# Optimization experiments

Measured on AMD Instinct MI355X. Metric: run time of the kernel, lower is better.

The kernel has to match this reference:

```python
import jax, jax.numpy as jnp
import numpy as np

N, QLEN, KLEN = 4, 2048, 2048
QDIM = KVDIM = 512
EMBED, HEADS = 1024, 16
HEAD_DIM = EMBED // HEADS


def setup_inputs() -> dict:
    key = jax.random.key(0)
    ks = jax.random.split(key, 7)
    return {
        "queries": jax.random.normal(ks[0], (N, QLEN, QDIM), dtype=jnp.float32),
        "keys": jax.random.normal(ks[1], (1, KLEN, KVDIM), dtype=jnp.float32),
        "values": jax.random.normal(ks[2], (1, KLEN, KVDIM), dtype=jnp.float32),
        "mask": jax.random.randint(ks[3], (N, 1, 1, KLEN), 0, 2, dtype=jnp.int32),
        "Wq": jax.random.normal(ks[4], (QDIM, EMBED), dtype=jnp.float32) * (QDIM ** -0.5),
        "Wk": jax.random.normal(ks[5], (KVDIM, EMBED), dtype=jnp.float32) * (KVDIM ** -0.5),
        "Wv": jax.random.normal(ks[6], (KVDIM, EMBED), dtype=jnp.float32) * (KVDIM ** -0.5),
    }


def reference(queries, keys, values, mask, Wq, Wk, Wv):
    # Projections (Linear, no bias)
    q = (queries @ Wq).reshape(N, QLEN, HEADS, HEAD_DIM)      # [N, Q, H, D]
    k = (keys @ Wk).reshape(KLEN, HEADS, HEAD_DIM)            # [K, H, D] (batch-1, shared)
    v = (values @ Wv).reshape(KLEN, HEADS, HEAD_DIM)          # [K, H, D]

    # energy: [N, H, Q, K]
    energy = jnp.einsum('nqhd,khd->nhqk', q, k)
    energy = jnp.where(mask == 0, jnp.float32(-1e20), energy)
    attn = jax.nn.softmax(energy / jnp.float32(HEAD_DIM ** 0.5), axis=3)

    out = jnp.einsum('nhqk,khd->nqhd', attn, v)               # [N, Q, H, D]
    return out.reshape(N, QLEN, EMBED)
```

## Files before the change

kernel.cpp:

```cpp
#include <hip/hip_runtime.h>

#define NB 4
#define QLEN 2048
#define KLEN 2048
#define QDIM 512
#define EMBED 1024
#define HEADS 16
#define HD 64

typedef __bf16 bf16x8 __attribute__((ext_vector_type(8)));
typedef float f32x4 __attribute__((ext_vector_type(4)));
typedef float f32x16 __attribute__((ext_vector_type(16)));

#define CLOG 0.18033688011112042f

__device__ __forceinline__ float fexp2(float x) {
#if __has_builtin(__builtin_amdgcn_exp2f)
    return __builtin_amdgcn_exp2f(x);
#else
    float r;
    asm("v_exp_f32 %0, %1\n\ts_nop 1" : "=v"(r) : "v"(x));
    return r;
#endif
}

#if __has_builtin(__builtin_amdgcn_sched_barrier)
#define SCHED_FENCE() __builtin_amdgcn_sched_barrier(0)
#else
#define SCHED_FENCE()
#endif

__device__ __forceinline__ void dma16(const void* g, void* l) {
    __builtin_amdgcn_global_load_lds(
        (const __attribute__((address_space(1))) void*)g,
        (__attribute__((address_space(3))) void*)l, 16, 0, 0);
}

__global__ __launch_bounds__(256) void prep(const float* __restrict__ q,
                                            const float* __restrict__ k,
                                            const float* __restrict__ v,
                                            const float* __restrict__ Wq,
                                            const float* __restrict__ Wk,
                                            const float* __restrict__ Wv,
                                            __bf16* __restrict__ qd,
                                            __bf16* __restrict__ kd,
                                            __bf16* __restrict__ vd,
                                            __bf16* __restrict__ WtQ,
                                            __bf16* __restrict__ WtK,
                                            __bf16* __restrict__ WtV) {
    __shared__ float tile[32][33];
    int b = blockIdx.x, tid = threadIdx.x;
    if (b < 3072) {
        const float* src; __bf16* dst; int cb;
        if (b < 2048)      { src = q; dst = qd; cb = b; }
        else if (b < 2560) { src = k; dst = kd; cb = b - 2048; }
        else               { src = v; dst = vd; cb = b - 2560; }
        int i = (cb * 256 + tid) * 8;
        float4 a0 = *(const float4*)&src[i];
        float4 a1 = *(const float4*)&src[i + 4];
        bf16x8 o;
        o[0] = (__bf16)a0.x; o[1] = (__bf16)a0.y; o[2] = (__bf16)a0.z; o[3] = (__bf16)a0.w;
        o[4] = (__bf16)a1.x; o[5] = (__bf16)a1.y; o[6] = (__bf16)a1.z; o[7] = (__bf16)a1.w;
        *(bf16x8*)&dst[i] = o;
    } else {
        int tb = b - 3072;
        int which = tb >> 9, r = tb & 511;
        const float* src = (which == 0) ? Wq : (which == 1) ? Wk : Wv;
        __bf16* dst = (which == 0) ? WtQ : (which == 1) ? WtK : WtV;
        float scale = (which == 0) ? CLOG : 1.0f;
        int e0 = (r & 31) * 32, c0 = (r >> 5) * 32;
        int tx = tid & 31, ty = tid >> 5;
        for (int i = 0; i < 4; i++)
            tile[ty + 8 * i][tx] = src[(c0 + ty + 8 * i) * EMBED + e0 + tx];
        __syncthreads();
        for (int i = 0; i < 4; i++)
            dst[(e0 + ty + 8 * i) * QDIM + c0 + tx] = (__bf16)(tile[tx][ty + 8 * i] * scale);
    }
}

__device__ __forceinline__ void gemm_compute(const __bf16* As, const __bf16* Bs,
                                             int wr, int wc, int r16, int qq,
                                             f32x4 (&acc)[4][4]) {
    bf16x8 af[4], bq[4];
#pragma unroll
    for (int i = 0; i < 4; i++)
        af[i] = *(const bf16x8*)&As[(wr * 64 + i * 16 + r16) * 32 + qq * 8];
#pragma unroll
    for (int j = 0; j < 4; j++)
        bq[j] = *(const bf16x8*)&Bs[(wc * 64 + j * 16 + r16) * 32 + qq * 8];
#pragma unroll
    for (int i = 0; i < 4; i++)
#pragma unroll
        for (int j = 0; j < 4; j++)
            acc[i][j] = __builtin_amdgcn_mfma_f32_16x16x32_bf16(af[i], bq[j], acc[i][j], 0, 0, 0);
}

__device__ __forceinline__ void gemm128(const __bf16* __restrict__ A,
                                        const __bf16* __restrict__ Bt,
                                        __bf16* As0, __bf16* As1,
                                        __bf16* Bs0, __bf16* Bs1,
                                        int row0, int col0, f32x4 (&acc)[4][4]) {
    int tid = threadIdx.x, wave = tid >> 6, lane = tid & 63;
    int r16 = lane & 15, qq = lane >> 4;
    int wr = wave >> 1, wc = wave & 1;
    const __bf16* agp1 = A + (size_t)(row0 + (tid >> 2)) * QDIM + (tid & 3) * 8;
    const __bf16* agp2 = A + (size_t)(row0 + 64 + (tid >> 2)) * QDIM + (tid & 3) * 8;
    const __bf16* bgp1 = Bt + (size_t)(col0 + (tid >> 2)) * QDIM + (tid & 3) * 8;
    const __bf16* bgp2 = Bt + (size_t)(col0 + 64 + (tid >> 2)) * QDIM + (tid & 3) * 8;
    __bf16 *a0a = &As0[wave * 512], *a0b = &As0[2048 + wave * 512];
    __bf16 *a1a = &As1[wave * 512], *a1b = &As1[2048 + wave * 512];
    __bf16 *b0a = &Bs0[wave * 512], *b0b = &Bs0[2048 + wave * 512];
    __bf16 *b1a = &Bs1[wave * 512], *b1b = &Bs1[2048 + wave * 512];

    dma16(agp1, a0a); dma16(agp2, a0b);
    dma16(bgp1, b0a); dma16(bgp2, b0b);
    agp1 += 32; agp2 += 32; bgp1 += 32; bgp2 += 32;
    __syncthreads();

    for (int t = 0; t < 16; t += 2) {
        dma16(agp1, a1a); dma16(agp2, a1b);
        dma16(bgp1, b1a); dma16(bgp2, b1b);
        agp1 += 32; agp2 += 32; bgp1 += 32; bgp2 += 32;
        SCHED_FENCE();
        gemm_compute(As0, Bs0, wr, wc, r16, qq, acc);
        __syncthreads();
        if (t + 2 < 16) {
            dma16(agp1, a0a); dma16(agp2, a0b);
            dma16(bgp1, b0a); dma16(bgp2, b0b);
            agp1 += 32; agp2 += 32; bgp1 += 32; bgp2 += 32;
        }
        SCHED_FENCE();
        gemm_compute(As1, Bs1, wr, wc, r16, qq, acc);
        __syncthreads();
    }
}

__global__ __launch_bounds__(256) void proj_all(const __bf16* __restrict__ qin,
                                                const __bf16* __restrict__ kin,
                                                const __bf16* __restrict__ vin,
                                                const __bf16* __restrict__ wtq,
                                                const __bf16* __restrict__ wtk,
                                                const __bf16* __restrict__ wtv,
                                                __bf16* __restrict__ qout,
                                                __bf16* __restrict__ kout,
                                                __bf16* __restrict__ vtout) {
    __shared__ __align__(16) __bf16 As[2][128 * 32];
    __shared__ __align__(16) __bf16 Bs[2][128 * 32];
    int bid = blockIdx.x;
    const __bf16 *A, *Bt;
    int mode, b;
    if (bid < 512)      { A = qin; Bt = wtq; mode = 0; b = bid; }
    else if (bid < 640) { A = kin; Bt = wtk; mode = 1; b = bid - 512; }
    else                { A = vin; Bt = wtv; mode = 2; b = bid - 640; }
    int row0 = (b >> 3) * 128, col0 = (b & 7) * 128;
    f32x4 acc[4][4] = {};
    gemm128(A, Bt, As[0], As[1], Bs[0], Bs[1], row0, col0, acc);
    int lane = threadIdx.x & 63, wave = threadIdx.x >> 6;
    int r16 = lane & 15, qq = lane >> 4;
    int wr = wave >> 1, wc = wave & 1;
#pragma unroll
    for (int i = 0; i < 4; i++)
#pragma unroll
        for (int j = 0; j < 4; j++)
#pragma unroll
            for (int rr = 0; rr < 4; rr++) {
                int grow = row0 + wr * 64 + i * 16 + qq * 4 + rr;
                int gcol = col0 + wc * 64 + j * 16 + r16;
                int hh = gcol >> 6, d = gcol & 63;
                __bf16 v = (__bf16)acc[i][j][rr];
                if (mode == 0) {
                    int n = grow >> 11, qr = grow & 2047;
                    qout[((size_t)(n * HEADS + hh) * QLEN + qr) * HD + d] = v;
                } else if (mode == 1) {
                    kout[((size_t)hh * KLEN + grow) * HD + d] = v;
                } else {
                    vtout[((size_t)hh * HD + d) * KLEN + grow] = v;
                }
            }
}

__device__ __forceinline__ void attn_tile(const __bf16* ksb, const __bf16* vsb,
                                          const float* mrow, const bf16x8 (&qfrag)[4],
                                          int col, int h,
                                          f32x16& o0, f32x16& o1, float& rsl) {
    bf16x8 pfrag[4];
#pragma unroll
    for (int kt2 = 0; kt2 < 2; kt2++) {
        int R = kt2 * 32 + col;
        f32x16 s = {};
#pragma unroll
        for (int c = 0; c < 4; c++) {
            int cc = (2 * c + h) ^ (R & 7);
            bf16x8 kf = *(const bf16x8*)&ksb[(R * 8 + cc) * 8];
            s = __builtin_amdgcn_mfma_f32_32x32x16_bf16(kf, qfrag[c], s, 0, 0, 0);
        }
#pragma unroll
        for (int G = 0; G < 4; G++) {
            f32x4 mt = *(const f32x4*)&mrow[kt2 * 32 + 16 * (G >> 1) + 8 * h + 4 * (G & 1)];
            int ci = 2 * kt2 + (G >> 1), e0 = (G & 1) * 4;
#pragma unroll
            for (int rr = 0; rr < 4; rr++) {
                float p = fexp2(s[4 * G + rr] + mt[rr]);
                rsl += p;
                pfrag[ci][e0 + rr] = (__bf16)p;
            }
        }
    }
#pragma unroll
    for (int c = 0; c < 4; c++) {
        int cc = (2 * c + h) ^ (col & 7);
        bf16x8 v0 = *(const bf16x8*)&vsb[(col * 8 + cc) * 8];
        bf16x8 v1 = *(const bf16x8*)&vsb[((32 + col) * 8 + cc) * 8];
        o0 = __builtin_amdgcn_mfma_f32_32x32x16_bf16(v0, pfrag[c], o0, 0, 0, 0);
        o1 = __builtin_amdgcn_mfma_f32_32x32x16_bf16(v1, pfrag[c], o1, 0, 0, 0);
    }
}

__global__ __launch_bounds__(256, 4) void attn_kernel(const __bf16* __restrict__ qb,
                                                      const __bf16* __restrict__ kb,
                                                      const __bf16* __restrict__ vtb,
                                                      const int* __restrict__ mask,
                                                      float* __restrict__ out) {
    __shared__ __align__(16) __bf16 ks[2][4096];
    __shared__ __align__(16) __bf16 vs[2][4096];
    __shared__ __align__(16) float msf[KLEN];

    int tid = threadIdx.x, wave = tid >> 6, lane = tid & 63;
    int col = lane & 31, h = lane >> 5;
    int q0 = blockIdx.x * 128, hh = blockIdx.y, n = blockIdx.z;
    const __bf16* qg = qb + ((size_t)(n * HEADS + hh) * QLEN + q0 + wave * 32 + col) * HD;
    const __bf16* kg = kb + (size_t)hh * KLEN * HD;
    const __bf16* vg = vtb + (size_t)hh * HD * KLEN;
    const int* mg = mask + n * KLEN;

    bf16x8 qfrag[4];
#pragma unroll
    for (int c = 0; c < 4; c++) qfrag[c] = *(const bf16x8*)&qg[c * 16 + h * 8];

    int s1 = tid, R1 = s1 >> 3, c1 = (s1 & 7) ^ (R1 & 7);
    int s2 = tid + 256, R2 = s2 >> 3, c2 = (s2 & 7) ^ (R2 & 7);
    int g1 = (R1 & 0x33) | ((R1 & 4) << 1) | ((R1 & 8) >> 1);
    int g2 = (R2 & 0x33) | ((R2 & 4) << 1) | ((R2 & 8) >> 1);
    const __bf16* kgp1 = kg + g1 * HD + c1 * 8;
    const __bf16* kgp2 = kg + g2 * HD + c2 * 8;
    const __bf16* vgp1 = vg + (size_t)R1 * KLEN + c1 * 8;
    const __bf16* vgp2 = vg + (size_t)R2 * KLEN + c2 * 8;
    __bf16 *kl0a = &ks[0][wave * 512], *kl0b = &ks[0][2048 + wave * 512];
    __bf16 *kl1a = &ks[1][wave * 512], *kl1b = &ks[1][2048 + wave * 512];
    __bf16 *vl0a = &vs[0][wave * 512], *vl0b = &vs[0][2048 + wave * 512];
    __bf16 *vl1a = &vs[1][wave * 512], *vl1b = &vs[1][2048 + wave * 512];

    dma16(kgp1, kl0a); dma16(kgp2, kl0b);
    dma16(vgp1, vl0a); dma16(vgp2, vl0b);
    kgp1 += 64 * HD; kgp2 += 64 * HD; vgp1 += 64; vgp2 += 64;
    {
        int i8 = tid * 8;
        int4 ma = *(const int4*)&mg[i8];
        int4 mb = *(const int4*)&mg[i8 + 4];
        f32x4 fa, fb;
        fa[0] = ma.x ? 0.f : -1e30f; fa[1] = ma.y ? 0.f : -1e30f;
        fa[2] = ma.z ? 0.f : -1e30f; fa[3] = ma.w ? 0.f : -1e30f;
        fb[0] = mb.x ? 0.f : -1e30f; fb[1] = mb.y ? 0.f : -1e30f;
        fb[2] = mb.z ? 0.f : -1e30f; fb[3] = mb.w ? 0.f : -1e30f;
        *(f32x4*)&msf[i8] = fa;
        *(f32x4*)&msf[i8 + 4] = fb;
    }
    __syncthreads();

    f32x16 o0 = {}, o1 = {};
    float rsl = 0.f;

    for (int t = 0; t < 32; t += 2) {
        dma16(kgp1, kl1a); dma16(kgp2, kl1b);
        dma16(vgp1, vl1a); dma16(vgp2, vl1b);
        kgp1 += 64 * HD; kgp2 += 64 * HD; vgp1 += 64; vgp2 += 64;
        SCHED_FENCE();
        attn_tile(ks[0], vs[0], &msf[t * 64], qfrag, col, h, o0, o1, rsl);
        __syncthreads();
        if (t + 2 < 32) {
            dma16(kgp1, kl0a); dma16(kgp2, kl0b);
            dma16(vgp1, vl0a); dma16(vgp2, vl0b);
            kgp1 += 64 * HD; kgp2 += 64 * HD; vgp1 += 64; vgp2 += 64;
        }
        SCHED_FENCE();
        attn_tile(ks[1], vs[1], &msf[(t + 1) * 64], qfrag, col, h, o0, o1, rsl);
        __syncthreads();
    }

    rsl += __shfl_xor(rsl, 32);
    float inv = 1.0f / rsl;
    float* op = out + ((size_t)n * QLEN + q0 + wave * 32 + col) * EMBED + hh * HD;
#pragma unroll
    for (int G = 0; G < 4; G++) {
        float4 t0, t1;
        t0.x = o0[4 * G + 0] * inv; t0.y = o0[4 * G + 1] * inv;
        t0.z = o0[4 * G + 2] * inv; t0.w = o0[4 * G + 3] * inv;
        t1.x = o1[4 * G + 0] * inv; t1.y = o1[4 * G + 1] * inv;
        t1.z = o1[4 * G + 2] * inv; t1.w = o1[4 * G + 3] * inv;
        *(float4*)&op[8 * G + 4 * h] = t0;
        *(float4*)&op[32 + 8 * G + 4 * h] = t1;
    }
}

extern "C" void kernel_launch(void* const* d_in, const int* in_sizes, int n_in,
                              void* d_out, int out_size, void* d_ws, size_t ws_size,
                              hipStream_t stream) {
    const float* queries = (const float*)d_in[0];
    const float* keys    = (const float*)d_in[1];
    const float* values  = (const float*)d_in[2];
    const int*   mask    = (const int*)d_in[3];
    const float* Wq      = (const float*)d_in[4];
    const float* Wk      = (const float*)d_in[5];
    const float* Wv      = (const float*)d_in[6];
    float* out = (float*)d_out;

    const size_t MiB = 1048576;
    char* ws = (char*)d_ws;
    __bf16* qbf   = (__bf16*)(ws);
    __bf16* kbf   = (__bf16*)(ws + 16 * MiB);
    __bf16* vtbf  = (__bf16*)(ws + 20 * MiB);
    __bf16* wtq   = (__bf16*)(ws + 24 * MiB);
    __bf16* wtk   = (__bf16*)(ws + 25 * MiB);
    __bf16* wtv   = (__bf16*)(ws + 26 * MiB);
    __bf16* qin   = (__bf16*)(ws + 27 * MiB);
    __bf16* kin   = (__bf16*)(ws + 35 * MiB);
    __bf16* vin   = (__bf16*)(ws + 37 * MiB);

    prep<<<4608, 256, 0, stream>>>(queries, keys, values, Wq, Wk, Wv,
                                   qin, kin, vin, wtq, wtk, wtv);
    proj_all<<<768, 256, 0, stream>>>(qin, kin, vin, wtq, wtk, wtv, qbf, kbf, vtbf);
    attn_kernel<<<dim3(QLEN / 128, HEADS, NB), 256, 0, stream>>>(qbf, kbf, vtbf, mask, out);
}
```

Before: 193.5 us.

## Compute V projection transposed directly, fold mask into MFMA init, add setprio

The V projection GEMM swaps its operands (Wv^T times values^T) so the output tile is already in the transposed head layout and can be written with contiguous stores, replacing the scattered transposing writes. In attention, the mask bias is loaded into the score accumulator before the QK MFMAs, removing the per-element add before exp2. Row sums are accumulated as packed 2-wide floats, and s_setprio raises wave priority around the MFMA sections. The risk is that the V path depends on gemm128 producing the correct layout with swapped operands and a changed grid tiling, and that setprio may not help scheduling.

```diff
diff --git a/kernel.cpp b/kernel.cpp
--- a/kernel.cpp
+++ b/kernel.cpp
@@ -9,6 +9,7 @@
 #define HD 64
 
 typedef __bf16 bf16x8 __attribute__((ext_vector_type(8)));
+typedef float f32x2 __attribute__((ext_vector_type(2)));
 typedef float f32x4 __attribute__((ext_vector_type(4)));
 typedef float f32x16 __attribute__((ext_vector_type(16)));
 
@@ -151,8 +152,10 @@
     int mode, b;
     if (bid < 512)      { A = qin; Bt = wtq; mode = 0; b = bid; }
     else if (bid < 640) { A = kin; Bt = wtk; mode = 1; b = bid - 512; }
-    else                { A = vin; Bt = wtv; mode = 2; b = bid - 640; }
-    int row0 = (b >> 3) * 128, col0 = (b & 7) * 128;
+    else                { A = wtv; Bt = vin; mode = 2; b = bid - 640; }
+    int row0, col0;
+    if (mode == 2) { row0 = (b >> 4) * 128; col0 = (b & 15) * 128; }
+    else           { row0 = (b >> 3) * 128; col0 = (b & 7) * 128; }
     f32x4 acc[4][4] = {};
     gemm128(A, Bt, As[0], As[1], Bs[0], Bs[1], row0, col0, acc);
     int lane = threadIdx.x & 63, wave = threadIdx.x >> 6;
@@ -166,15 +169,16 @@
             for (int rr = 0; rr < 4; rr++) {
                 int grow = row0 + wr * 64 + i * 16 + qq * 4 + rr;
                 int gcol = col0 + wc * 64 + j * 16 + r16;
-                int hh = gcol >> 6, d = gcol & 63;
                 __bf16 v = (__bf16)acc[i][j][rr];
                 if (mode == 0) {
+                    int hh = gcol >> 6, d = gcol & 63;
                     int n = grow >> 11, qr = grow & 2047;
                     qout[((size_t)(n * HEADS + hh) * QLEN + qr) * HD + d] = v;
                 } else if (mode == 1) {
+                    int hh = gcol >> 6, d = gcol & 63;
                     kout[((size_t)hh * KLEN + grow) * HD + d] = v;
                 } else {
-                    vtout[((size_t)hh * HD + d) * KLEN + grow] = v;
+                    vtout[(size_t)grow * KLEN + gcol] = v;
                 }
             }
 }
@@ -182,30 +186,39 @@
 __device__ __forceinline__ void attn_tile(const __bf16* ksb, const __bf16* vsb,
                                           const float* mrow, const bf16x8 (&qfrag)[4],
                                           int col, int h,
-                                          f32x16& o0, f32x16& o1, float& rsl) {
+                                          f32x16& o0, f32x16& o1, f32x2& rsl) {
     bf16x8 pfrag[4];
 #pragma unroll
     for (int kt2 = 0; kt2 < 2; kt2++) {
         int R = kt2 * 32 + col;
-        f32x16 s = {};
+        union { f32x16 v; f32x4 q[4]; } su;
+#pragma unroll
+        for (int G = 0; G < 4; G++)
+            su.q[G] = *(const f32x4*)&mrow[kt2 * 32 + 16 * (G >> 1) + 8 * h + 4 * (G & 1)];
+        f32x16 s = su.v;
+        __builtin_amdgcn_s_setprio(1);
 #pragma unroll
         for (int c = 0; c < 4; c++) {
             int cc = (2 * c + h) ^ (R & 7);
             bf16x8 kf = *(const bf16x8*)&ksb[(R * 8 + cc) * 8];
             s = __builtin_amdgcn_mfma_f32_32x32x16_bf16(kf, qfrag[c], s, 0, 0, 0);
         }
+        __builtin_amdgcn_s_setprio(0);
 #pragma unroll
         for (int G = 0; G < 4; G++) {
-            f32x4 mt = *(const f32x4*)&mrow[kt2 * 32 + 16 * (G >> 1) + 8 * h + 4 * (G & 1)];
             int ci = 2 * kt2 + (G >> 1), e0 = (G & 1) * 4;
 #pragma unroll
-            for (int rr = 0; rr < 4; rr++) {
-                float p = fexp2(s[4 * G + rr] + mt[rr]);
-                rsl += p;
-                pfrag[ci][e0 + rr] = (__bf16)p;
+            for (int rr = 0; rr < 4; rr += 2) {
+                float p0 = fexp2(s[4 * G + rr]);
+                float p1 = fexp2(s[4 * G + rr + 1]);
+                f32x2 pp; pp[0] = p0; pp[1] = p1;
+                rsl += pp;
+                pfrag[ci][e0 + rr] = (__bf16)p0;
+                pfrag[ci][e0 + rr + 1] = (__bf16)p1;
             }
         }
     }
+    __builtin_amdgcn_s_setprio(1);
 #pragma unroll
     for (int c = 0; c < 4; c++) {
         int cc = (2 * c + h) ^ (col & 7);
@@ -214,6 +227,7 @@
         o0 = __builtin_amdgcn_mfma_f32_32x32x16_bf16(v0, pfrag[c], o0, 0, 0, 0);
         o1 = __builtin_amdgcn_mfma_f32_32x32x16_bf16(v1, pfrag[c], o1, 0, 0, 0);
     }
+    __builtin_amdgcn_s_setprio(0);
 }
 
 __global__ __launch_bounds__(256, 4) void attn_kernel(const __bf16* __restrict__ qb,
@@ -268,7 +282,7 @@
     __syncthreads();
 
     f32x16 o0 = {}, o1 = {};
-    float rsl = 0.f;
+    f32x2 rsl = {};
 
     for (int t = 0; t < 32; t += 2) {
         dma16(kgp1, kl1a); dma16(kgp2, kl1b);
@@ -287,8 +301,9 @@
         __syncthreads();
     }
 
-    rsl += __shfl_xor(rsl, 32);
-    float inv = 1.0f / rsl;
+    float rs = rsl[0] + rsl[1];
+    rs += __shfl_xor(rs, 32);
+    float inv = 1.0f / rs;
     float* op = out + ((size_t)n * QLEN + q0 + wave * 32 + col) * EMBED + hh * HD;
 #pragma unroll
     for (int G = 0; G < 4; G++) {
```

New measurement: 184.1 us. 4.9% less time.
